# Kernel optimization log

Hardware: AMD Instinct MI355X
Metric: run time of the kernel (lower is better)

The kernel has to match this reference:

```python
import jax, jax.numpy as jnp
from jax import lax
import numpy as np

B, E, K, C, H, G, D = 2048, 8, 2, 100, 1024, 2048, 2048  # batch, experts, top_k, classes, mlp_hidden, gate_hidden, feat_dim


def setup_inputs() -> dict:
    key = jax.random.key(0)
    ks = jax.random.split(key, 24)
    f32 = jnp.float32

    def n(k, shape, s=0.05):
        return jax.random.normal(k, shape, f32) * s

    inp = {
        "x": jax.random.normal(ks[0], (B, 3, 32, 32), f32),
        "noise": jax.random.normal(ks[1], (B, E), f32),
        # CifarConv params (BN in eval mode: running mean 0 / var 1 folded into bn())
        "cw1": n(ks[2], (64, 3, 3, 3)), "cb1": jnp.zeros((64,), f32), "g1": jnp.ones((64,), f32), "be1": jnp.zeros((64,), f32),
        "cw2": n(ks[3], (128, 64, 3, 3)), "cb2": jnp.zeros((128,), f32), "g2": jnp.ones((128,), f32), "be2": jnp.zeros((128,), f32),
        "cw3": n(ks[4], (256, 128, 3, 3)), "cb3": jnp.zeros((256,), f32), "g3": jnp.ones((256,), f32), "be3": jnp.zeros((256,), f32),
        "cw4": n(ks[5], (512, 256, 3, 3)), "cb4": jnp.zeros((512,), f32), "g4": jnp.ones((512,), f32), "be4": jnp.zeros((512,), f32),
        # gating nets (Linear->ReLU->Linear)
        "wg1": n(ks[6], (D, G), 0.02), "wg1b": jnp.zeros((G,), f32),
        "wg2": n(ks[7], (G, E), 0.02), "wg2b": jnp.zeros((E,), f32),
        "wn1": n(ks[8], (D, G), 0.02), "wn1b": jnp.zeros((G,), f32),
        "wn2": n(ks[9], (G, E), 0.02), "wn2b": jnp.zeros((E,), f32),
        # stacked expert MLPs 2048->1024->512->100
        "eW1": n(ks[10], (E, D, H), 0.02), "eb1": jnp.zeros((E, H), f32),
        "eW2": n(ks[11], (E, H, H // 2), 0.02), "eb2": jnp.zeros((E, H // 2), f32),
        "eW3": n(ks[12], (E, H // 2, C), 0.02), "eb3": jnp.zeros((E, C), f32),
    }
    return inp


def reference(x, noise, cw1, cb1, g1, be1, cw2, cb2, g2, be2, cw3, cb3, g3, be3,
              cw4, cb4, g4, be4, wg1, wg1b, wg2, wg2b, wn1, wn1b, wn2, wn2b,
              eW1, eb1, eW2, eb2, eW3, eb3):
    def conv(h, w, b):
        return lax.conv_general_dilated(h, w, (1, 1), "SAME",
                                        dimension_numbers=("NCHW", "OIHW", "NCHW")) + b[None, :, None, None]

    def bn(h, g, b):  # eval-mode BN with running mean 0, var 1
        return h * (g / jnp.sqrt(1.0 + 1e-5))[None, :, None, None] + b[None, :, None, None]

    def pool(h):
        return lax.reduce_window(h, -jnp.inf, lax.max, (1, 1, 2, 2), (1, 1, 2, 2), "VALID")

    h = pool(jax.nn.relu(bn(conv(x, cw1, cb1), g1, be1)))
    h = pool(jax.nn.relu(bn(conv(h, cw2, cb2), g2, be2)))
    h = pool(jax.nn.relu(bn(conv(h, cw3, cb3), g3, be3)))
    h = pool(jax.nn.relu(bn(conv(h, cw4, cb4), g4, be4)))
    f = h.reshape(h.shape[0], 512 * 2 * 2)  # [B, 2048]

    # noisy top-k gating
    clean = jax.nn.relu(f @ wg1 + wg1b) @ wg2 + wg2b           # [B, E]
    raw_std = jax.nn.relu(f @ wn1 + wn1b) @ wn2 + wn2b
    std = jax.nn.softplus(raw_std) + 0.01                      # noise_epsilon
    noisy = clean + noise * std
    logits = noisy

    topv, topi = lax.top_k(logits, K + 1)                      # [B, K+1]
    topk_gates = jax.nn.softmax(topv[:, :K], axis=1)           # softmax over top-k logits
    rows = jnp.arange(logits.shape[0])[:, None]
    gates = jnp.zeros_like(logits).at[rows, topi[:, :K]].set(topk_gates)  # [B, E]

    # differentiable load (_prob_in_top_k)
    th_in = topv[:, K][:, None]
    th_out = topv[:, K - 1][:, None]
    ncdf = lambda z: 0.5 * (1.0 + lax.erf(z / jnp.sqrt(jnp.float32(2.0))))
    prob = jnp.where(noisy > th_in, ncdf((clean - th_in) / std), ncdf((clean - th_out) / std))
    load = prob.sum(0)                                         # [E]
    importance = gates.sum(0)                                  # [E]

    def cv2(v):
        return jnp.var(v, ddof=1) / (jnp.mean(v) ** 2 + 1e-10)

    loss = cv2(importance) + cv2(load)

    # dispatch/combine == dense gate-weighted mixture (gate==0 rows contribute 0)
    eh = jax.nn.relu(jnp.einsum("bd,edh->ebh", f, eW1) + eb1[:, None, :])
    eh = jax.nn.relu(jnp.einsum("ebh,ehg->ebg", eh, eW2) + eb2[:, None, :])
    eo = jnp.einsum("ebg,egc->ebc", eh, eW3) + eb3[:, None, :]  # [E, B, C]
    y = jnp.einsum("be,ebc->bc", gates, eo)                     # [B, C]
    return y, loss
```

## Files before the change

### kernel.cpp

```cpp
#include <hip/hip_runtime.h>

#define BB 2048
#define EE 8
#define CC 100

typedef __attribute__((ext_vector_type(8))) short s16x8;
typedef __attribute__((ext_vector_type(4))) float f32x4;

__device__ inline ushort f2b(float f) {
    union { float f; unsigned u; } c; c.f = f;
    return (ushort)((c.u + 0x7fffu + ((c.u >> 16) & 1u)) >> 16);
}
__device__ inline float b2f(ushort h) {
    union { unsigned u; float f; } c; c.u = ((unsigned)h) << 16;
    return c.f;
}

__global__ __launch_bounds__(256) void zero_ws_kernel(int4* __restrict__ p, long n16)
{
    long i = (long)blockIdx.x * 256 + threadIdx.x;
    const long stride = (long)gridDim.x * 256;
    const int4 z = make_int4(0, 0, 0, 0);
    for (; i < n16; i += stride) p[i] = z;
}

__global__ __launch_bounds__(256) void conv1_kernel(
    const float* __restrict__ x, const float* __restrict__ w,
    const float* __restrict__ cb, const float* __restrict__ g,
    const float* __restrict__ be, float* __restrict__ out)
{
    __shared__ float xs[3][34][34];
    __shared__ float wsm[64][28];
    __shared__ float sc_s[64], bi_s[64];

    const int b = blockIdx.x;
    const int tid = threadIdx.x;

    for (int i = tid; i < 3 * 34 * 34; i += 256) {
        int ci = i / (34 * 34);
        int r  = (i / 34) % 34;
        int c  = i % 34;
        float v = 0.f;
        if (r >= 1 && r <= 32 && c >= 1 && c <= 32)
            v = x[(((long)b * 3 + ci) * 32 + (r - 1)) * 32 + (c - 1)];
        xs[ci][r][c] = v;
    }
    for (int i = tid; i < 64 * 27; i += 256) {
        int co = i / 27, k = i % 27;
        wsm[co][k] = w[co * 27 + k];
    }
    if (tid < 64) {
        float s = g[tid] * 0.99999500003749969f;
        sc_s[tid] = s;
        bi_s[tid] = cb[tid] * s + be[tid];
    }
    __syncthreads();

    const int py = tid >> 4, px = tid & 15;
    float xr[3][4][4];
    #pragma unroll
    for (int ci = 0; ci < 3; ci++)
        #pragma unroll
        for (int r = 0; r < 4; r++)
            #pragma unroll
            for (int c = 0; c < 4; c++)
                xr[ci][r][c] = xs[ci][2 * py + r][2 * px + c];

    for (int co = 0; co < 64; co++) {
        float a0 = 0.f, a1 = 0.f, a2 = 0.f, a3 = 0.f;
        #pragma unroll
        for (int ci = 0; ci < 3; ci++)
            #pragma unroll
            for (int ky = 0; ky < 3; ky++)
                #pragma unroll
                for (int kx = 0; kx < 3; kx++) {
                    float wv = wsm[co][ci * 9 + ky * 3 + kx];
                    a0 += wv * xr[ci][ky][kx];
                    a1 += wv * xr[ci][ky][kx + 1];
                    a2 += wv * xr[ci][ky + 1][kx];
                    a3 += wv * xr[ci][ky + 1][kx + 1];
                }
        float s = sc_s[co], bb2 = bi_s[co];
        float v0 = fmaxf(a0 * s + bb2, 0.f);
        float v1 = fmaxf(a1 * s + bb2, 0.f);
        float v2 = fmaxf(a2 * s + bb2, 0.f);
        float v3 = fmaxf(a3 * s + bb2, 0.f);
        float v  = fmaxf(fmaxf(v0, v1), fmaxf(v2, v3));
        out[(((long)b * 16 + py) * 16 + px) * 64 + co] = v;
    }
}

__global__ void prep_convw(const float* __restrict__ w, ushort* __restrict__ oh,
                           ushort* __restrict__ ol, int CO, int CI)
{
    long total = (long)CO * CI * 9;
    long i = (long)blockIdx.x * 256 + threadIdx.x;
    if (i >= total) return;
    int co = (int)(i / (9 * CI));
    int rem = (int)(i % (9 * CI));
    int s = rem / CI, ci = rem % CI;
    float v = w[((long)co * CI + ci) * 9 + s];
    ushort h = f2b(v);
    long o = (long)co * (9 * CI) + (long)s * CI + ci;
    oh[o] = h;
    ol[o] = f2b(v - b2f(h));
}

template <bool SPLIT>
__global__ __launch_bounds__(256) void prep_wT(
    const float* __restrict__ in, ushort* __restrict__ oh, ushort* __restrict__ ol,
    int K, int N, int Npad)
{
    __shared__ float tile[32][33];
    const int b = blockIdx.z;
    in += (long)b * K * N;
    oh += (long)b * Npad * K;
    if (SPLIT) ol += (long)b * Npad * K;
    const int k0 = blockIdx.y * 32, n0 = blockIdx.x * 32;
    const int tx = threadIdx.x & 31, ty = threadIdx.x >> 5;
    for (int i = ty; i < 32; i += 8) {
        int k = k0 + i, n = n0 + tx;
        tile[i][tx] = (k < K && n < N) ? in[(long)k * N + n] : 0.f;
    }
    __syncthreads();
    for (int i = ty; i < 32; i += 8) {
        int n = n0 + i, k = k0 + tx;
        if (n < Npad && k < K) {
            float v = tile[tx][i];
            ushort h = f2b(v);
            oh[(long)n * K + k] = h;
            if (SPLIT) ol[(long)n * K + k] = f2b(v - b2f(h));
        }
    }
}

__global__ void prep_bias2(const float* __restrict__ a, const float* __restrict__ b,
                           float* __restrict__ o)
{
    int i = blockIdx.x * 256 + threadIdx.x;
    if (i < 2048) o[i] = a[i];
    else if (i < 4096) o[i] = b[i - 2048];
}

template <int ASRC, int EPI, bool SPLIT, bool RELU, int S, int CI>
__global__ __launch_bounds__(256) void mgemm(
    const float* __restrict__ Agf,
    const ushort* __restrict__ Ah, const ushort* __restrict__ Al,
    const ushort* __restrict__ Bh, const ushort* __restrict__ Bl,
    const float* __restrict__ bias,
    const float* __restrict__ cbp, const float* __restrict__ gp,
    const float* __restrict__ bep,
    void* __restrict__ O1, ushort* __restrict__ O2,
    int M, int N, int K, int realN,
    long aStr, long bStr, long biasStr, long oStr)
{
    constexpr int BKp = 40;
    __shared__ ushort sAh[128 * BKp];
    __shared__ ushort sBh[128 * BKp];
    __shared__ ushort sAl[SPLIT ? 128 * BKp : 8];
    __shared__ ushort sBl[SPLIT ? 128 * BKp : 8];

    const int e = blockIdx.z;
    if constexpr (ASRC == 0) {
        Ah += (long)e * aStr;
        if (SPLIT) Al += (long)e * aStr;
    }
    Bh += (long)e * bStr;
    if (SPLIT) Bl += (long)e * bStr;
    bias += (long)e * biasStr;

    const int tid = threadIdx.x;
    const int bm = blockIdx.x * 128, bn = blockIdx.y * 128;
    const int lane = tid & 63, wid = tid >> 6;
    const int wm0 = (wid >> 1) * 64, wn0 = (wid & 1) * 64;
    const int l16 = lane & 15, gq = lane >> 4;
    const int koff = gq * 8;

    int g_im = 0, g_y0 = 0, g_x0 = 0;
    const int sr = tid >> 1, scb = (tid & 1) * 16;
    if constexpr (ASRC == 1) {
        int p = bm + sr;
        g_im = p / (S * S);
        int rem = p % (S * S);
        g_y0 = rem / S;
        g_x0 = rem % S;
    }

    f32x4 acc[4][4];
    #pragma unroll
    for (int i = 0; i < 4; ++i)
        #pragma unroll
        for (int j = 0; j < 4; ++j)
            acc[i][j] = (f32x4){0.f, 0.f, 0.f, 0.f};

    for (int k0 = 0; k0 < K; k0 += 32) {
        __syncthreads();
        if constexpr (ASRC == 1) {
            const int s = k0 / CI, ci0 = k0 % CI;
            const int yy = g_y0 + s / 3 - 1, xx = g_x0 + (s % 3) - 1;
            const bool ok = (yy >= 0) && (yy < S) && (xx >= 0) && (xx < S);
            const float* src = Agf + ((((long)g_im * S + yy) * S + xx) * CI + ci0 + scb);
            #pragma unroll
            for (int q = 0; q < 4; ++q) {
                float4 v = ok ? ((const float4*)src)[q]
                              : make_float4(0.f, 0.f, 0.f, 0.f);
                ushort4 hv, lv;
                hv.x = f2b(v.x); hv.y = f2b(v.y); hv.z = f2b(v.z); hv.w = f2b(v.w);
                lv.x = f2b(v.x - b2f(hv.x)); lv.y = f2b(v.y - b2f(hv.y));
                lv.z = f2b(v.z - b2f(hv.z)); lv.w = f2b(v.w - b2f(hv.w));
                int o = sr * BKp + scb + q * 4;
                *(ushort4*)&sAh[o] = hv;
                *(ushort4*)&sAl[o] = lv;
            }
        } else {
            #pragma unroll
            for (int i2 = 0; i2 < 2; ++i2) {
                int c = tid + i2 * 256;
                int r = c >> 2, cb = (c & 3) * 8;
                *(int4*)&sAh[r * BKp + cb] = *(const int4*)&Ah[(long)(bm + r) * K + k0 + cb];
                if (SPLIT)
                    *(int4*)&sAl[r * BKp + cb] = *(const int4*)&Al[(long)(bm + r) * K + k0 + cb];
            }
        }
        #pragma unroll
        for (int i2 = 0; i2 < 2; ++i2) {
            int c = tid + i2 * 256;
            int r = c >> 2, cb = (c & 3) * 8;
            *(int4*)&sBh[r * BKp + cb] = *(const int4*)&Bh[(long)(bn + r) * K + k0 + cb];
            if (SPLIT)
                *(int4*)&sBl[r * BKp + cb] = *(const int4*)&Bl[(long)(bn + r) * K + k0 + cb];
        }
        __syncthreads();

        s16x8 fa[4], fb[4], fal[4], fbl[4];
        #pragma unroll
        for (int i = 0; i < 4; ++i) {
            fa[i] = *(const s16x8*)&sAh[(wm0 + i * 16 + l16) * BKp + koff];
            fb[i] = *(const s16x8*)&sBh[(wn0 + i * 16 + l16) * BKp + koff];
            if (SPLIT) {
                fal[i] = *(const s16x8*)&sAl[(wm0 + i * 16 + l16) * BKp + koff];
                fbl[i] = *(const s16x8*)&sBl[(wn0 + i * 16 + l16) * BKp + koff];
            }
        }
        #pragma unroll
        for (int i = 0; i < 4; ++i)
            #pragma unroll
            for (int j = 0; j < 4; ++j) {
                acc[i][j] = __builtin_amdgcn_mfma_f32_16x16x32_bf16(fa[i], fb[j], acc[i][j], 0, 0, 0);
                if (SPLIT) {
                    acc[i][j] = __builtin_amdgcn_mfma_f32_16x16x32_bf16(fa[i],  fbl[j], acc[i][j], 0, 0, 0);
                    acc[i][j] = __builtin_amdgcn_mfma_f32_16x16x32_bf16(fal[i], fb[j],  acc[i][j], 0, 0, 0);
                }
            }
    }

    if constexpr (EPI == 3) {
        const int pbase = bm + wm0;
        if constexpr (S == 16) {
            const int im = pbase / 256;
            const int yb = (pbase % 256) / 16;
            #pragma unroll
            for (int ip = 0; ip < 2; ++ip)
                #pragma unroll
                for (int j = 0; j < 4; ++j) {
                    const int n = bn + wn0 + j * 16 + l16;
                    const float sc = gp[n] * 0.99999500003749969f;
                    const float bi = cbp[n] * sc + bep[n];
                    #pragma unroll
                    for (int rp = 0; rp < 2; ++rp) {
                        float a00 = fmaxf(acc[2*ip][j][2*rp]     * sc + bi, 0.f);
                        float a01 = fmaxf(acc[2*ip][j][2*rp + 1] * sc + bi, 0.f);
                        float a10 = fmaxf(acc[2*ip+1][j][2*rp]     * sc + bi, 0.f);
                        float a11 = fmaxf(acc[2*ip+1][j][2*rp + 1] * sc + bi, 0.f);
                        float pv = fmaxf(fmaxf(a00, a01), fmaxf(a10, a11));
                        const int py = yb / 2 + ip;
                        const int px = gq * 2 + rp;
                        ((float*)O1)[((long)(im * 8 + py) * 8 + px) * N + n] = pv;
                    }
                }
        } else {
            const int im = pbase / 64;
            #pragma unroll
            for (int i = 0; i < 4; ++i)
                #pragma unroll
                for (int j = 0; j < 4; ++j) {
                    const int n = bn + wn0 + j * 16 + l16;
                    const float sc = gp[n] * 0.99999500003749969f;
                    const float bi = cbp[n] * sc + bep[n];
                    #pragma unroll
                    for (int rp = 0; rp < 2; ++rp) {
                        float xa = fmaxf(acc[i][j][2*rp]     * sc + bi, 0.f);
                        float xb = fmaxf(acc[i][j][2*rp + 1] * sc + bi, 0.f);
                        float xm = fmaxf(xa, xb);
                        float ym = fmaxf(xm, __shfl_xor(xm, 32));
                        if (lane < 32) {
                            const int py = i, px = (gq & 1) * 2 + rp;
                            ((float*)O1)[((long)(im * 4 + py) * 4 + px) * N + n] = ym;
                        }
                    }
                }
        }
    } else if constexpr (EPI == 4) {
        const int pbase = bm + wm0;
        const int im0 = pbase / 16;
        #pragma unroll
        for (int i = 0; i < 4; ++i)
            #pragma unroll
            for (int j = 0; j < 4; ++j) {
                const int n = bn + wn0 + j * 16 + l16;
                const float sc = gp[n] * 0.99999500003749969f;
                const float bi = cbp[n] * sc + bep[n];
                #pragma unroll
                for (int rp = 0; rp < 2; ++rp) {
                    float xa = fmaxf(acc[i][j][2*rp]     * sc + bi, 0.f);
                    float xb = fmaxf(acc[i][j][2*rp + 1] * sc + bi, 0.f);
                    float xm = fmaxf(xa, xb);
                    float ym = fmaxf(xm, __shfl_xor(xm, 16));
                    if ((gq & 1) == 0) {
                        const int py = gq >> 1, px = rp;
                        const long fi = (long)(im0 + i) * 2048 + (long)n * 4 + py * 2 + px;
                        ushort h = f2b(ym);
                        ((ushort*)O1)[fi] = h;
                        O2[fi] = f2b(ym - b2f(h));
                    }
                }
            }
    } else {
        #pragma unroll
        for (int i = 0; i < 4; ++i)
            #pragma unroll
            for (int j = 0; j < 4; ++j) {
                const int n = bn + wn0 + j * 16 + l16;
                const float bv = (n < realN) ? bias[n] : 0.f;
                #pragma unroll
                for (int r = 0; r < 4; ++r) {
                    const int m = bm + wm0 + i * 16 + gq * 4 + r;
                    float v = acc[i][j][r] + bv;
                    if (RELU) v = fmaxf(v, 0.f);
                    if constexpr (EPI == 1)
                        ((ushort*)O1 + (long)e * oStr)[(long)m * N + n] = f2b(v);
                    else
                        ((float*)O1 + (long)e * oStr)[(long)m * N + n] = v;
                }
            }
    }
}

__global__ __launch_bounds__(256) void small2_kernel(
    const float* __restrict__ gh, const float* __restrict__ wg2,
    const float* __restrict__ wg2b, const float* __restrict__ wn2,
    const float* __restrict__ wn2b, float* __restrict__ clean,
    float* __restrict__ rawp)
{
    const int b = blockIdx.x, tid = threadIdx.x;
    float ac[8] = {0,0,0,0,0,0,0,0}, ar[8] = {0,0,0,0,0,0,0,0};
    for (int k = tid; k < 2048; k += 256) {
        float a1 = gh[(long)b * 4096 + k];
        float a2 = gh[(long)b * 4096 + 2048 + k];
        const float4* w1 = (const float4*)&wg2[(long)k * 8];
        float4 p = w1[0], q = w1[1];
        ac[0] += a1 * p.x; ac[1] += a1 * p.y; ac[2] += a1 * p.z; ac[3] += a1 * p.w;
        ac[4] += a1 * q.x; ac[5] += a1 * q.y; ac[6] += a1 * q.z; ac[7] += a1 * q.w;
        const float4* w2 = (const float4*)&wn2[(long)k * 8];
        p = w2[0]; q = w2[1];
        ar[0] += a2 * p.x; ar[1] += a2 * p.y; ar[2] += a2 * p.z; ar[3] += a2 * p.w;
        ar[4] += a2 * q.x; ar[5] += a2 * q.y; ar[6] += a2 * q.z; ar[7] += a2 * q.w;
    }
    __shared__ float red[256][16];
    #pragma unroll
    for (int e2 = 0; e2 < 8; e2++) { red[tid][e2] = ac[e2]; red[tid][8 + e2] = ar[e2]; }
    __syncthreads();
    for (int s = 128; s > 0; s >>= 1) {
        if (tid < s)
            #pragma unroll
            for (int e2 = 0; e2 < 16; e2++) red[tid][e2] += red[tid + s][e2];
        __syncthreads();
    }
    if (tid < 8) clean[(long)b * 8 + tid] = red[0][tid] + wg2b[tid];
    else if (tid < 16) rawp[(long)b * 8 + tid - 8] = red[0][tid] + wn2b[tid - 8];
}

__global__ __launch_bounds__(256) void gate_kernel(
    const float* __restrict__ clean, const float* __restrict__ raw,
    const float* __restrict__ noise, float* __restrict__ gates,
    float* __restrict__ part)
{
    __shared__ float red[256][8];
    const int tid = threadIdx.x;
    const int b = blockIdx.x * 256 + tid;

    float cl[8], st[8], ny[8];
    #pragma unroll
    for (int e2 = 0; e2 < 8; e2++) {
        cl[e2] = clean[(long)b * 8 + e2];
        float r = raw[(long)b * 8 + e2];
        st[e2] = fmaxf(r, 0.f) + log1pf(expf(-fabsf(r))) + 0.01f;
        ny[e2] = cl[e2] + noise[(long)b * 8 + e2] * st[e2];
    }
    float v0 = -3e38f, v1 = -3e38f, v2 = -3e38f;
    int i0 = 0, i1 = 0;
    #pragma unroll
    for (int e2 = 0; e2 < 8; e2++) {
        float xv = ny[e2];
        if (xv > v0)      { v2 = v1; v1 = v0; i1 = i0; v0 = xv; i0 = e2; }
        else if (xv > v1) { v2 = v1; v1 = xv; i1 = e2; }
        else if (xv > v2) { v2 = xv; }
    }
    float e1 = expf(v1 - v0);
    float z  = 1.f + e1;
    float g0 = 1.f / z, g1 = e1 / z;

    const float inv_sqrt2 = 0.70710678118654752f;
    float grow[8], prob[8];
    #pragma unroll
    for (int e2 = 0; e2 < 8; e2++) {
        grow[e2] = (e2 == i0) ? g0 : ((e2 == i1) ? g1 : 0.f);
        float th = (ny[e2] > v2) ? v2 : v1;
        float zz = (cl[e2] - th) / st[e2];
        prob[e2] = 0.5f * (1.f + erff(zz * inv_sqrt2));
        gates[(long)b * 8 + e2] = grow[e2];
    }
    #pragma unroll
    for (int e2 = 0; e2 < 8; e2++) red[tid][e2] = grow[e2];
    __syncthreads();
    for (int s = 128; s > 0; s >>= 1) {
        if (tid < s)
            #pragma unroll
            for (int e2 = 0; e2 < 8; e2++) red[tid][e2] += red[tid + s][e2];
        __syncthreads();
    }
    if (tid < 8) part[blockIdx.x * 16 + tid] = red[0][tid];
    __syncthreads();
    #pragma unroll
    for (int e2 = 0; e2 < 8; e2++) red[tid][e2] = prob[e2];
    __syncthreads();
    for (int s = 128; s > 0; s >>= 1) {
        if (tid < s)
            #pragma unroll
            for (int e2 = 0; e2 < 8; e2++) red[tid][e2] += red[tid + s][e2];
        __syncthreads();
    }
    if (tid < 8) part[blockIdx.x * 16 + 8 + tid] = red[0][tid];
}

__global__ void loss_kernel(const float* __restrict__ part, float* __restrict__ lossp)
{
    if (threadIdx.x == 0) {
        float imp[8], ld[8];
        for (int e2 = 0; e2 < 8; e2++) { imp[e2] = 0.f; ld[e2] = 0.f; }
        for (int blk = 0; blk < 8; blk++)
            for (int e2 = 0; e2 < 8; e2++) {
                imp[e2] += part[blk * 16 + e2];
                ld[e2]  += part[blk * 16 + 8 + e2];
            }
        float mi = 0.f, ml = 0.f;
        for (int e2 = 0; e2 < 8; e2++) { mi += imp[e2]; ml += ld[e2]; }
        mi *= 0.125f; ml *= 0.125f;
        float vi = 0.f, vl = 0.f;
        for (int e2 = 0; e2 < 8; e2++) {
            vi += (imp[e2] - mi) * (imp[e2] - mi);
            vl += (ld[e2] - ml) * (ld[e2] - ml);
        }
        vi /= 7.f; vl /= 7.f;
        lossp[0] = vi / (mi * mi + 1e-10f) + vl / (ml * ml + 1e-10f);
    }
}

__global__ void combine_kernel(const float* __restrict__ gates,
                               const float* __restrict__ eo, float* __restrict__ y)
{
    const int idx = blockIdx.x * 256 + threadIdx.x;
    if (idx >= BB * CC) return;
    const int b = idx / CC, c = idx % CC;
    float s = 0.f;
    #pragma unroll
    for (int e2 = 0; e2 < 8; e2++)
        s += gates[(long)b * 8 + e2] * eo[((long)e2 * BB + b) * 128 + c];
    y[idx] = s;
}

extern "C" void kernel_launch(void* const* d_in, const int* in_sizes, int n_in,
                              void* d_out, int out_size, void* d_ws, size_t ws_size,
                              hipStream_t stream)
{
    const float* x     = (const float*)d_in[0];
    const float* noise = (const float*)d_in[1];
    const float* cw1 = (const float*)d_in[2];  const float* cb1 = (const float*)d_in[3];
    const float* g1  = (const float*)d_in[4];  const float* be1 = (const float*)d_in[5];
    const float* cw2 = (const float*)d_in[6];  const float* cb2 = (const float*)d_in[7];
    const float* g2  = (const float*)d_in[8];  const float* be2 = (const float*)d_in[9];
    const float* cw3 = (const float*)d_in[10]; const float* cb3 = (const float*)d_in[11];
    const float* g3  = (const float*)d_in[12]; const float* be3 = (const float*)d_in[13];
    const float* cw4 = (const float*)d_in[14]; const float* cb4 = (const float*)d_in[15];
    const float* g4  = (const float*)d_in[16]; const float* be4 = (const float*)d_in[17];
    const float* wg1 = (const float*)d_in[18]; const float* wg1b = (const float*)d_in[19];
    const float* wg2 = (const float*)d_in[20]; const float* wg2b = (const float*)d_in[21];
    const float* wn1 = (const float*)d_in[22]; const float* wn1b = (const float*)d_in[23];
    const float* wn2 = (const float*)d_in[24]; const float* wn2b = (const float*)d_in[25];
    const float* eW1 = (const float*)d_in[26]; const float* eb1 = (const float*)d_in[27];
    const float* eW2 = (const float*)d_in[28]; const float* eb2 = (const float*)d_in[29];
    const float* eW3 = (const float*)d_in[30]; const float* eb3 = (const float*)d_in[31];

    float* out = (float*)d_out;
    char*  W   = (char*)d_ws;

    zero_ws_kernel<<<4096, 256, 0, stream>>>((int4*)d_ws, (long)(ws_size / 16));

    float*  c2    = (float*) (W + 0);
    float*  c3in  = (float*) (W + 134217728);
    float*  c4in  = (float*) (W + 0);
    ushort* fh    = (ushort*)(W + 33554432);
    ushort* fl    = (ushort*)(W + 41943040);
    ushort* wTh   = (ushort*)(W + 50331648);
    ushort* wTl   = (ushort*)(W + 67108864);
    float*  bias4096 = (float*)(W + 83886080);
    float*  gh    = (float*) (W + 83902464);
    float*  clean = (float*) (W + 117456896);
    float*  rawp  = (float*) (W + 117522432);
    float*  gates = (float*) (W + 117587968);
    float*  part  = (float*) (W + 117653504);
    ushort* eW1T  = (ushort*)(W + 134217728);
    ushort* eW2T  = (ushort*)(W + 167772160);
    ushort* eW3T  = (ushort*)(W + 176160768);
    ushort* eh1   = (ushort*)(W + 177209344);
    ushort* eh2   = (ushort*)(W + 83902464);
    float*  eo    = (float*) (W + 0);
    ushort* bc2h  = (ushort*)(W + 210763776);
    ushort* bc2l  = (ushort*)(W + 210911232);
    ushort* bc3h  = (ushort*)(W + 211058688);
    ushort* bc3l  = (ushort*)(W + 211648512);
    ushort* bc4h  = (ushort*)(W + 212238336);
    ushort* bc4l  = (ushort*)(W + 214597632);

    prep_convw<<<(9 * 128 * 64 + 255) / 256, 256, 0, stream>>>(cw2, bc2h, bc2l, 128, 64);
    prep_convw<<<(9 * 256 * 128 + 255) / 256, 256, 0, stream>>>(cw3, bc3h, bc3l, 256, 128);
    prep_convw<<<(9 * 512 * 256 + 255) / 256, 256, 0, stream>>>(cw4, bc4h, bc4l, 512, 256);

    conv1_kernel<<<2048, 256, 0, stream>>>(x, cw1, cb1, g1, be1, c2);
    mgemm<1, 3, true, false, 16, 64><<<dim3(4096, 1), 256, 0, stream>>>(
        c2, nullptr, nullptr, bc2h, bc2l, nullptr, cb2, g2, be2,
        c3in, nullptr, 524288, 128, 576, 128, 0, 0, 0, 0);

    prep_wT<true><<<dim3(64, 64, 1), 256, 0, stream>>>(wg1, wTh, wTl, 2048, 2048, 2048);
    prep_wT<true><<<dim3(64, 64, 1), 256, 0, stream>>>(wn1, wTh + 4194304, wTl + 4194304, 2048, 2048, 2048);
    prep_bias2<<<16, 256, 0, stream>>>(wg1b, wn1b, bias4096);

    mgemm<1, 3, true, false, 8, 128><<<dim3(1024, 2), 256, 0, stream>>>(
        c3in, nullptr, nullptr, bc3h, bc3l, nullptr, cb3, g3, be3,
        c4in, nullptr, 131072, 256, 1152, 256, 0, 0, 0, 0);

    prep_wT<false><<<dim3(32, 64, 8), 256, 0, stream>>>(eW1, eW1T, nullptr, 2048, 1024, 1024);
    prep_wT<false><<<dim3(16, 32, 8), 256, 0, stream>>>(eW2, eW2T, nullptr, 1024, 512, 512);
    prep_wT<false><<<dim3(4, 16, 8), 256, 0, stream>>>(eW3, eW3T, nullptr, 512, 100, 128);

    mgemm<1, 4, true, false, 4, 256><<<dim3(256, 4), 256, 0, stream>>>(
        c4in, nullptr, nullptr, bc4h, bc4l, nullptr, cb4, g4, be4,
        fh, fl, 32768, 512, 2304, 512, 0, 0, 0, 0);

    mgemm<0, 0, true, true, 1, 1><<<dim3(16, 32, 1), 256, 0, stream>>>(
        nullptr, fh, fl, wTh, wTl, bias4096, nullptr, nullptr, nullptr,
        gh, nullptr, 2048, 4096, 2048, 4096, 0, 0, 0, 0);
    small2_kernel<<<BB, 256, 0, stream>>>(gh, wg2, wg2b, wn2, wn2b, clean, rawp);
    gate_kernel<<<8, 256, 0, stream>>>(clean, rawp, noise, gates, part);
    loss_kernel<<<1, 64, 0, stream>>>(part, out + (long)BB * CC);

    mgemm<0, 1, false, true, 1, 1><<<dim3(16, 8, 8), 256, 0, stream>>>(
        nullptr, fh, nullptr, eW1T, nullptr, eb1, nullptr, nullptr, nullptr,
        eh1, nullptr, 2048, 1024, 2048, 1024, 0, (long)1024 * 2048, 1024, (long)2048 * 1024);
    mgemm<0, 1, false, true, 1, 1><<<dim3(16, 4, 8), 256, 0, stream>>>(
        nullptr, eh1, nullptr, eW2T, nullptr, eb2, nullptr, nullptr, nullptr,
        eh2, nullptr, 2048, 512, 1024, 512, (long)2048 * 1024, (long)512 * 1024, 512, (long)2048 * 512);
    mgemm<0, 2, false, false, 1, 1><<<dim3(16, 1, 8), 256, 0, stream>>>(
        nullptr, eh2, nullptr, eW3T, nullptr, eb3, nullptr, nullptr, nullptr,
        eo, nullptr, 2048, 128, 512, 100, (long)2048 * 512, (long)128 * 512, 100, (long)2048 * 128);

    combine_kernel<<<(BB * CC + 255) / 256, 256, 0, stream>>>(gates, eo, out);
}
```

Measured before the change: 1.685 ms.

## Store conv activations as split bf16 and register-prefetch GEMM tiles

Conv epilogues now write activations as hi/lo bf16 pairs instead of fp32, so the implicit-GEMM conv loads use 16-byte int4 copies without per-tile conversion. The GEMM main loop prefetches the next K-tile into registers while computing the current one, and launch bounds request 4 blocks per CU. The workspace zeroing is limited to the used region. This adds register pressure from the prefetch buffers, and the launch-bound hint may force spills.

```diff
diff --git a/kernel.cpp b/kernel.cpp
--- a/kernel.cpp
+++ b/kernel.cpp
@@ -27,7 +27,7 @@
 __global__ __launch_bounds__(256) void conv1_kernel(
     const float* __restrict__ x, const float* __restrict__ w,
     const float* __restrict__ cb, const float* __restrict__ g,
-    const float* __restrict__ be, float* __restrict__ out)
+    const float* __restrict__ be, ushort* __restrict__ oh, ushort* __restrict__ ol)
 {
     __shared__ float xs[3][34][34];
     __shared__ float wsm[64][28];
@@ -86,7 +86,10 @@
         float v2 = fmaxf(a2 * s + bb2, 0.f);
         float v3 = fmaxf(a3 * s + bb2, 0.f);
         float v  = fmaxf(fmaxf(v0, v1), fmaxf(v2, v3));
-        out[(((long)b * 16 + py) * 16 + px) * 64 + co] = v;
+        long o = (((long)b * 16 + py) * 16 + px) * 64 + co;
+        ushort h = f2b(v);
+        oh[o] = h;
+        ol[o] = f2b(v - b2f(h));
     }
 }
 
@@ -143,8 +146,8 @@
 }
 
 template <int ASRC, int EPI, bool SPLIT, bool RELU, int S, int CI>
-__global__ __launch_bounds__(256) void mgemm(
-    const float* __restrict__ Agf,
+__global__ __launch_bounds__(256, 4) void mgemm(
+    const ushort* __restrict__ Agh, const ushort* __restrict__ Agl,
     const ushort* __restrict__ Ah, const ushort* __restrict__ Al,
     const ushort* __restrict__ Bh, const ushort* __restrict__ Bl,
     const float* __restrict__ bias,
@@ -176,8 +179,10 @@
     const int l16 = lane & 15, gq = lane >> 4;
     const int koff = gq * 8;
 
+    const int r0 = tid >> 2, cb = (tid & 3) * 8;
+    const int sr = tid >> 1, scb = (tid & 1) * 16;
+
     int g_im = 0, g_y0 = 0, g_x0 = 0;
-    const int sr = tid >> 1, scb = (tid & 1) * 16;
     if constexpr (ASRC == 1) {
         int p = bm + sr;
         g_im = p / (S * S);
@@ -186,6 +191,52 @@
         g_x0 = rem % S;
     }
 
+    int4 rah0, rah1, ral0, ral1, rbh0, rbh1, rbl0, rbl1;
+
+    auto loadT = [&](int k0) {
+        if constexpr (ASRC == 1) {
+            const int s = k0 / CI, ci0 = k0 % CI;
+            const int yy = g_y0 + s / 3 - 1, xx = g_x0 + (s % 3) - 1;
+            if (yy >= 0 && yy < S && xx >= 0 && xx < S) {
+                const long base = (((long)g_im * S + yy) * S + xx) * CI + ci0 + scb;
+                rah0 = *(const int4*)&Agh[base];
+                rah1 = *(const int4*)&Agh[base + 8];
+                ral0 = *(const int4*)&Agl[base];
+                ral1 = *(const int4*)&Agl[base + 8];
+            } else {
+                rah0 = rah1 = ral0 = ral1 = make_int4(0, 0, 0, 0);
+            }
+        } else {
+            rah0 = *(const int4*)&Ah[(long)(bm + r0) * K + k0 + cb];
+            rah1 = *(const int4*)&Ah[(long)(bm + r0 + 64) * K + k0 + cb];
+            if (SPLIT) {
+                ral0 = *(const int4*)&Al[(long)(bm + r0) * K + k0 + cb];
+                ral1 = *(const int4*)&Al[(long)(bm + r0 + 64) * K + k0 + cb];
+            }
+        }
+        rbh0 = *(const int4*)&Bh[(long)(bn + r0) * K + k0 + cb];
+        rbh1 = *(const int4*)&Bh[(long)(bn + r0 + 64) * K + k0 + cb];
+        if (SPLIT) {
+            rbl0 = *(const int4*)&Bl[(long)(bn + r0) * K + k0 + cb];
+            rbl1 = *(const int4*)&Bl[(long)(bn + r0 + 64) * K + k0 + cb];
+        }
+    };
+
+    auto writeT = [&]() {
+        if constexpr (ASRC == 1) {
+            int o = sr * BKp + scb;
+            *(int4*)&sAh[o] = rah0; *(int4*)&sAh[o + 8] = rah1;
+            *(int4*)&sAl[o] = ral0; *(int4*)&sAl[o + 8] = ral1;
+        } else {
+            int oa = r0 * BKp + cb;
+            *(int4*)&sAh[oa] = rah0; *(int4*)&sAh[oa + 64 * BKp] = rah1;
+            if (SPLIT) { *(int4*)&sAl[oa] = ral0; *(int4*)&sAl[oa + 64 * BKp] = ral1; }
+        }
+        int ob = r0 * BKp + cb;
+        *(int4*)&sBh[ob] = rbh0; *(int4*)&sBh[ob + 64 * BKp] = rbh1;
+        if (SPLIT) { *(int4*)&sBl[ob] = rbl0; *(int4*)&sBl[ob + 64 * BKp] = rbl1; }
+    };
+
     f32x4 acc[4][4];
     #pragma unroll
     for (int i = 0; i < 4; ++i)
@@ -193,43 +244,11 @@
         for (int j = 0; j < 4; ++j)
             acc[i][j] = (f32x4){0.f, 0.f, 0.f, 0.f};
 
+    loadT(0);
     for (int k0 = 0; k0 < K; k0 += 32) {
         __syncthreads();
-        if constexpr (ASRC == 1) {
-            const int s = k0 / CI, ci0 = k0 % CI;
-            const int yy = g_y0 + s / 3 - 1, xx = g_x0 + (s % 3) - 1;
-            const bool ok = (yy >= 0) && (yy < S) && (xx >= 0) && (xx < S);
-            const float* src = Agf + ((((long)g_im * S + yy) * S + xx) * CI + ci0 + scb);
-            #pragma unroll
-            for (int q = 0; q < 4; ++q) {
-                float4 v = ok ? ((const float4*)src)[q]
-                              : make_float4(0.f, 0.f, 0.f, 0.f);
-                ushort4 hv, lv;
-                hv.x = f2b(v.x); hv.y = f2b(v.y); hv.z = f2b(v.z); hv.w = f2b(v.w);
-                lv.x = f2b(v.x - b2f(hv.x)); lv.y = f2b(v.y - b2f(hv.y));
-                lv.z = f2b(v.z - b2f(hv.z)); lv.w = f2b(v.w - b2f(hv.w));
-                int o = sr * BKp + scb + q * 4;
-                *(ushort4*)&sAh[o] = hv;
-                *(ushort4*)&sAl[o] = lv;
-            }
-        } else {
-            #pragma unroll
-            for (int i2 = 0; i2 < 2; ++i2) {
-                int c = tid + i2 * 256;
-                int r = c >> 2, cb = (c & 3) * 8;
-                *(int4*)&sAh[r * BKp + cb] = *(const int4*)&Ah[(long)(bm + r) * K + k0 + cb];
-                if (SPLIT)
-                    *(int4*)&sAl[r * BKp + cb] = *(const int4*)&Al[(long)(bm + r) * K + k0 + cb];
-            }
-        }
-        #pragma unroll
-        for (int i2 = 0; i2 < 2; ++i2) {
-            int c = tid + i2 * 256;
-            int r = c >> 2, cb = (c & 3) * 8;
-            *(int4*)&sBh[r * BKp + cb] = *(const int4*)&Bh[(long)(bn + r) * K + k0 + cb];
-            if (SPLIT)
-                *(int4*)&sBl[r * BKp + cb] = *(const int4*)&Bl[(long)(bn + r) * K + k0 + cb];
-        }
+        writeT();
+        if (k0 + 32 < K) loadT(k0 + 32);
         __syncthreads();
 
         s16x8 fa[4], fb[4], fal[4], fbl[4];
@@ -275,7 +294,10 @@
                         float pv = fmaxf(fmaxf(a00, a01), fmaxf(a10, a11));
                         const int py = yb / 2 + ip;
                         const int px = gq * 2 + rp;
-                        ((float*)O1)[((long)(im * 8 + py) * 8 + px) * N + n] = pv;
+                        long idx = ((long)(im * 8 + py) * 8 + px) * N + n;
+                        ushort h = f2b(pv);
+                        ((ushort*)O1)[idx] = h;
+                        O2[idx] = f2b(pv - b2f(h));
                     }
                 }
         } else {
@@ -295,7 +317,10 @@
                         float ym = fmaxf(xm, __shfl_xor(xm, 32));
                         if (lane < 32) {
                             const int py = i, px = (gq & 1) * 2 + rp;
-                            ((float*)O1)[((long)(im * 4 + py) * 4 + px) * N + n] = ym;
+                            long idx = ((long)(im * 4 + py) * 4 + px) * N + n;
+                            ushort h = f2b(ym);
+                            ((ushort*)O1)[idx] = h;
+                            O2[idx] = f2b(ym - b2f(h));
                         }
                     }
                 }
@@ -504,11 +529,12 @@
     float* out = (float*)d_out;
     char*  W   = (char*)d_ws;
 
-    zero_ws_kernel<<<4096, 256, 0, stream>>>((int4*)d_ws, (long)(ws_size / 16));
-
-    float*  c2    = (float*) (W + 0);
-    float*  c3in  = (float*) (W + 134217728);
-    float*  c4in  = (float*) (W + 0);
+    ushort* c2h   = (ushort*)(W + 0);
+    ushort* c2l   = (ushort*)(W + 67108864);
+    ushort* c3h   = (ushort*)(W + 134217728);
+    ushort* c3l   = (ushort*)(W + 167772160);
+    ushort* c4h   = (ushort*)(W + 0);
+    ushort* c4l   = (ushort*)(W + 16777216);
     ushort* fh    = (ushort*)(W + 33554432);
     ushort* fl    = (ushort*)(W + 41943040);
     ushort* wTh   = (ushort*)(W + 50331648);
@@ -532,46 +558,52 @@
     ushort* bc4h  = (ushort*)(W + 212238336);
     ushort* bc4l  = (ushort*)(W + 214597632);
 
+    {
+        long used = 216956928;
+        long cap = (ws_size < (size_t)used) ? (long)ws_size : used;
+        zero_ws_kernel<<<2048, 256, 0, stream>>>((int4*)d_ws, cap / 16);
+    }
+
     prep_convw<<<(9 * 128 * 64 + 255) / 256, 256, 0, stream>>>(cw2, bc2h, bc2l, 128, 64);
     prep_convw<<<(9 * 256 * 128 + 255) / 256, 256, 0, stream>>>(cw3, bc3h, bc3l, 256, 128);
     prep_convw<<<(9 * 512 * 256 + 255) / 256, 256, 0, stream>>>(cw4, bc4h, bc4l, 512, 256);
 
-    conv1_kernel<<<2048, 256, 0, stream>>>(x, cw1, cb1, g1, be1, c2);
+    conv1_kernel<<<2048, 256, 0, stream>>>(x, cw1, cb1, g1, be1, c2h, c2l);
     mgemm<1, 3, true, false, 16, 64><<<dim3(4096, 1), 256, 0, stream>>>(
-        c2, nullptr, nullptr, bc2h, bc2l, nullptr, cb2, g2, be2,
-        c3in, nullptr, 524288, 128, 576, 128, 0, 0, 0, 0);
+        c2h, c2l, nullptr, nullptr, bc2h, bc2l, nullptr, cb2, g2, be2,
+        c3h, c3l, 524288, 128, 576, 128, 0, 0, 0, 0);
 
     prep_wT<true><<<dim3(64, 64, 1), 256, 0, stream>>>(wg1, wTh, wTl, 2048, 2048, 2048);
     prep_wT<true><<<dim3(64, 64, 1), 256, 0, stream>>>(wn1, wTh + 4194304, wTl + 4194304, 2048, 2048, 2048);
     prep_bias2<<<16, 256, 0, stream>>>(wg1b, wn1b, bias4096);
 
     mgemm<1, 3, true, false, 8, 128><<<dim3(1024, 2), 256, 0, stream>>>(
-        c3in, nullptr, nullptr, bc3h, bc3l, nullptr, cb3, g3, be3,
-        c4in, nullptr, 131072, 256, 1152, 256, 0, 0, 0, 0);
+        c3h, c3l, nullptr, nullptr, bc3h, bc3l, nullptr, cb3, g3, be3,
+        c4h, c4l, 131072, 256, 1152, 256, 0, 0, 0, 0);
 
     prep_wT<false><<<dim3(32, 64, 8), 256, 0, stream>>>(eW1, eW1T, nullptr, 2048, 1024, 1024);
     prep_wT<false><<<dim3(16, 32, 8), 256, 0, stream>>>(eW2, eW2T, nullptr, 1024, 512, 512);
     prep_wT<false><<<dim3(4, 16, 8), 256, 0, stream>>>(eW3, eW3T, nullptr, 512, 100, 128);
 
     mgemm<1, 4, true, false, 4, 256><<<dim3(256, 4), 256, 0, stream>>>(
-        c4in, nullptr, nullptr, bc4h, bc4l, nullptr, cb4, g4, be4,
+        c4h, c4l, nullptr, nullptr, bc4h, bc4l, nullptr, cb4, g4, be4,
         fh, fl, 32768, 512, 2304, 512, 0, 0, 0, 0);
 
     mgemm<0, 0, true, true, 1, 1><<<dim3(16, 32, 1), 256, 0, stream>>>(
-        nullptr, fh, fl, wTh, wTl, bias4096, nullptr, nullptr, nullptr,
+        nullptr, nullptr, fh, fl, wTh, wTl, bias4096, nullptr, nullptr, nullptr,
         gh, nullptr, 2048, 4096, 2048, 4096, 0, 0, 0, 0);
     small2_kernel<<<BB, 256, 0, stream>>>(gh, wg2, wg2b, wn2, wn2b, clean, rawp);
     gate_kernel<<<8, 256, 0, stream>>>(clean, rawp, noise, gates, part);
     loss_kernel<<<1, 64, 0, stream>>>(part, out + (long)BB * CC);
 
     mgemm<0, 1, false, true, 1, 1><<<dim3(16, 8, 8), 256, 0, stream>>>(
-        nullptr, fh, nullptr, eW1T, nullptr, eb1, nullptr, nullptr, nullptr,
+        nullptr, nullptr, fh, nullptr, eW1T, nullptr, eb1, nullptr, nullptr, nullptr,
         eh1, nullptr, 2048, 1024, 2048, 1024, 0, (long)1024 * 2048, 1024, (long)2048 * 1024);
     mgemm<0, 1, false, true, 1, 1><<<dim3(16, 4, 8), 256, 0, stream>>>(
-        nullptr, eh1, nullptr, eW2T, nullptr, eb2, nullptr, nullptr, nullptr,
+        nullptr, nullptr, eh1, nullptr, eW2T, nullptr, eb2, nullptr, nullptr, nullptr,
         eh2, nullptr, 2048, 512, 1024, 512, (long)2048 * 1024, (long)512 * 1024, 512, (long)2048 * 512);
     mgemm<0, 2, false, false, 1, 1><<<dim3(16, 1, 8), 256, 0, stream>>>(
-        nullptr, eh2, nullptr, eW3T, nullptr, eb3, nullptr, nullptr, nullptr,
+        nullptr, nullptr, eh2, nullptr, eW3T, nullptr, eb3, nullptr, nullptr, nullptr,
         eo, nullptr, 2048, 128, 512, 100, (long)2048 * 512, (long)128 * 512, 100, (long)2048 * 128);
 
     combine_kernel<<<(BB * CC + 255) / 256, 256, 0, stream>>>(gates, eo, out);
```

After: 4.395 ms. 2.61x slower.
